# Optimization experiments

Hardware: AMD Instinct MI355X
Metric: run time of the kernel (lower is better)

## Reference

```python
import jax, jax.numpy as jnp
import numpy as np

N = 100000
E = 1600000
IN_DIM = 256
HID = 64


def setup_inputs() -> dict:
    key = jax.random.key(0)
    k1, k2, k3 = jax.random.split(key, 3)
    x = jax.random.normal(k1, (N, IN_DIM), dtype=jnp.float32)
    edge_index = jax.random.randint(k2, (2, E), 0, N, dtype=jnp.int64)
    # glorot-ish init for GCNConv weight, zero bias (PyG default)
    W = jax.random.normal(k3, (IN_DIM, HID), dtype=jnp.float32) * (1.0 / np.sqrt(IN_DIM))
    b = jnp.zeros((HID,), dtype=jnp.float32)
    return {"x": x, "edge_index": edge_index, "W": W, "b": b}


def reference(x, edge_index, W, b):
    # GCNConv: out = D^{-1/2} (A + I) D^{-1/2} (X W) + b
    n = x.shape[0]
    # add self-loops
    loop = jnp.arange(n, dtype=edge_index.dtype)
    src = jnp.concatenate([edge_index[0], loop])  # [E+N]
    dst = jnp.concatenate([edge_index[1], loop])  # [E+N]
    # degree of target nodes (incl. self-loops)
    deg = jax.ops.segment_sum(jnp.ones_like(dst, dtype=x.dtype), dst, num_segments=n)
    dinv = jnp.where(deg > 0, jax.lax.rsqrt(deg), 0.0)  # deg^{-1/2}, inf->0
    norm = dinv[src] * dinv[dst]  # [E+N]
    h = x @ W  # [N, HID] transform before aggregation
    msg = h[src] * norm[:, None]  # gather + scale, [E+N, HID]
    out = jax.ops.segment_sum(msg, dst, num_segments=n)  # scatter-add
    return out + b
```

## Files before the change

kernel.cpp:

```cpp
#include <hip/hip_runtime.h>

typedef float floatx4 __attribute__((ext_vector_type(4)));
typedef short s16x8 __attribute__((ext_vector_type(8)));

#define WG 256
#define NBUCK 512
#define BSH 8
#define EBLK 512
#define CAP 8192
#define MAXIT 16

__device__ inline unsigned pack_bf16_rne(float a, float b) {
    unsigned ua = __float_as_uint(a), ub = __float_as_uint(b);
    ua = (ua + 0x7FFFu + ((ua >> 16) & 1u)) >> 16;
    ub = (ub + 0x7FFFu + ((ub >> 16) & 1u)) >> 16;
    return ua | (ub << 16);
}

union FragU {
    unsigned u[4];
    uint4 q;
    s16x8 v;
};

__global__ __launch_bounds__(WG) void k_packw(const float* __restrict__ W,
                                              uint4* __restrict__ wpack,
                                              int* __restrict__ cursor) {
    const int q = blockIdx.x * WG + threadIdx.x;
    if (q < NBUCK) cursor[q] = 0;
    const int kb = q >> 8, nt = (q >> 6) & 3, ln = q & 63;
    const int quad = ln >> 4, l15 = ln & 15;
    const int col = nt * 16 + l15;
    const int krow = kb * 32 + quad * 8;
    unsigned up[4];
#pragma unroll
    for (int p = 0; p < 4; p++) {
        float a = W[(krow + 2 * p) * 64 + col];
        float b2 = W[(krow + 2 * p + 1) * 64 + col];
        up[p] = pack_bf16_rne(a, b2);
    }
    uint4 pk = {up[0], up[1], up[2], up[3]};
    wpack[q] = pk;
}

__global__ __launch_bounds__(WG, 4) void k_main(const void* __restrict__ ei, int* __restrict__ cursor,
                                                unsigned* __restrict__ ebuf, int E,
                                                const float* __restrict__ x, const uint4* __restrict__ wpack,
                                                unsigned short* __restrict__ g, int N) {
    __shared__ int hh[NBUCK];
    __shared__ int hbase[NBUCK];
    __shared__ int s32flag;
    const int t = threadIdx.x;

    if ((int)blockIdx.x < EBLK) {
        if (t == 0) s32flag = 0;
        for (int i = t; i < NBUCK; i += WG) hh[i] = 0;
        __syncthreads();
        {
            const int* w = (const int*)ei;
            int nz = 0;
            for (int j = t; j < 4096; j += WG) nz |= (w[2 * j + 1] != 0);
            if (nz) atomicOr(&s32flag, 1);
        }
        __syncthreads();
        const bool i32 = (s32flag != 0);
        const int chunk = (E + EBLK - 1) / EBLK;
        const int s = blockIdx.x * chunk;
        const int eend = min(E, s + chunk);

        if (chunk <= MAXIT * WG) {
            unsigned ew[MAXIT];
            unsigned short ebk[MAXIT];
#pragma unroll
            for (int i = 0; i < MAXIT; i++) {
                const int e = s + t + i * WG;
                ebk[i] = 0xFFFFu;
                if (e < eend) {
                    int sN, dN;
                    if (i32) {
                        const int* p = (const int*)ei;
                        sN = p[e];
                        dN = p[E + e];
                    } else {
                        const long long* p = (const long long*)ei;
                        sN = (int)p[e];
                        dN = (int)p[(long long)E + e];
                    }
                    ew[i] = (unsigned)sN | ((unsigned)(dN & 255) << 24);
                    ebk[i] = (unsigned short)(dN >> BSH);
                    atomicAdd(&hh[dN >> BSH], 1);
                }
            }
            __syncthreads();
            for (int i = t; i < NBUCK; i += WG) {
                int c = hh[i];
                hbase[i] = c ? atomicAdd(&cursor[i], c) : 0;
                hh[i] = 0;
            }
            __syncthreads();
#pragma unroll
            for (int i = 0; i < MAXIT; i++) {
                if (ebk[i] != 0xFFFFu) {
                    const int bkt = ebk[i];
                    const int pos = hbase[bkt] + atomicAdd(&hh[bkt], 1);
                    if (pos < CAP) ebuf[(size_t)bkt * CAP + pos] = ew[i];
                }
            }
        } else {
            if (i32) {
                const int* pd = (const int*)ei + E;
                for (int e = s + t; e < eend; e += WG) atomicAdd(&hh[pd[e] >> BSH], 1);
            } else {
                const long long* pd = (const long long*)ei + E;
                for (int e = s + t; e < eend; e += WG) atomicAdd(&hh[(int)pd[e] >> BSH], 1);
            }
            __syncthreads();
            for (int i = t; i < NBUCK; i += WG) {
                int c = hh[i];
                hbase[i] = c ? atomicAdd(&cursor[i], c) : 0;
                hh[i] = 0;
            }
            __syncthreads();
            for (int e = s + t; e < eend; e += WG) {
                int sN, dN;
                if (i32) {
                    const int* p = (const int*)ei;
                    sN = p[e];
                    dN = p[E + e];
                } else {
                    const long long* p = (const long long*)ei;
                    sN = (int)p[e];
                    dN = (int)p[(long long)E + e];
                }
                int bkt = dN >> BSH;
                int pos = hbase[bkt] + atomicAdd(&hh[bkt], 1);
                if (pos < CAP) ebuf[(size_t)bkt * CAP + pos] = (unsigned)sN | ((unsigned)(dN & 255) << 24);
            }
        }
    } else {
        const int bb = blockIdx.x - EBLK;
        const int wv = t >> 6;
        const int lane = t & 63;
        const int quad = lane >> 4, l15 = lane & 15;

        long long arow = (long long)bb * 64 + wv * 16 + l15;
        if (arow >= N) arow = N - 1;
        const float* xr = x + arow * 256 + quad * 8;
        const uint4* wp = wpack + lane;

        floatx4 xv[8][2];
#pragma unroll
        for (int kb = 0; kb < 8; kb++) {
            xv[kb][0] = *(const floatx4*)(xr + kb * 32);
            xv[kb][1] = *(const floatx4*)(xr + kb * 32 + 4);
        }
#pragma unroll
        for (int kb = 0; kb < 8; kb++) {
            asm volatile("" : "+v"(xv[kb][0]), "+v"(xv[kb][1]));
        }
        __builtin_amdgcn_sched_barrier(0);

        floatx4 acc[4];
#pragma unroll
        for (int nt = 0; nt < 4; nt++) acc[nt] = 0.f;

        FragU bc0, bc1, bc2, bc3;
        bc0.q = wp[0 * 64];
        bc1.q = wp[1 * 64];
        bc2.q = wp[2 * 64];
        bc3.q = wp[3 * 64];

#pragma unroll
        for (int kb = 0; kb < 8; kb++) {
            FragU bn0, bn1, bn2, bn3;
            if (kb < 7) {
                bn0.q = wp[((kb + 1) * 4 + 0) * 64];
                bn1.q = wp[((kb + 1) * 4 + 1) * 64];
                bn2.q = wp[((kb + 1) * 4 + 2) * 64];
                bn3.q = wp[((kb + 1) * 4 + 3) * 64];
            }
            FragU a;
            a.u[0] = pack_bf16_rne(xv[kb][0][0], xv[kb][0][1]);
            a.u[1] = pack_bf16_rne(xv[kb][0][2], xv[kb][0][3]);
            a.u[2] = pack_bf16_rne(xv[kb][1][0], xv[kb][1][1]);
            a.u[3] = pack_bf16_rne(xv[kb][1][2], xv[kb][1][3]);
            acc[0] = __builtin_amdgcn_mfma_f32_16x16x32_bf16(a.v, bc0.v, acc[0], 0, 0, 0);
            acc[1] = __builtin_amdgcn_mfma_f32_16x16x32_bf16(a.v, bc1.v, acc[1], 0, 0, 0);
            acc[2] = __builtin_amdgcn_mfma_f32_16x16x32_bf16(a.v, bc2.v, acc[2], 0, 0, 0);
            acc[3] = __builtin_amdgcn_mfma_f32_16x16x32_bf16(a.v, bc3.v, acc[3], 0, 0, 0);
            if (kb < 7) {
                bc0 = bn0;
                bc1 = bn1;
                bc2 = bn2;
                bc3 = bn3;
            }
        }

        const long long orow0 = (long long)bb * 64 + wv * 16 + quad * 4;
#pragma unroll
        for (int r = 0; r < 4; r++) {
            const long long orow = orow0 + r;
            if (orow < N) {
#pragma unroll
                for (int nt = 0; nt < 4; nt++) {
                    float v = acc[nt][r];
                    unsigned uv = __float_as_uint(v);
                    uv = (uv + 0x7FFFu + ((uv >> 16) & 1u)) >> 16;
                    g[orow * 64 + nt * 16 + l15] = (unsigned short)uv;
                }
            }
        }
    }
}

__global__ __launch_bounds__(WG) void k_csr(const unsigned* __restrict__ ebuf, const int* __restrict__ cursor,
                                            int* __restrict__ off, int* __restrict__ srcs,
                                            float* __restrict__ dinv, int N, int nbuse) {
    __shared__ int red[256];
    __shared__ int h[256];
    __shared__ int sc[256];
    __shared__ int cur[256];
    const int t = threadIdx.x;
    const int b = blockIdx.x;
    const int node0 = b << BSH;
    const int rows = min(256, N - node0);
    int part = 0;
    for (int i = t; i < b; i += WG) part += min(cursor[i], CAP);
    red[t] = part;
    h[t] = 0;
    __syncthreads();
    for (int d = WG / 2; d > 0; d >>= 1) {
        if (t < d) red[t] += red[t + d];
        __syncthreads();
    }
    const int ebase = red[0];
    const int cnt = min(cursor[b], CAP);
    const unsigned* eb = ebuf + (size_t)b * CAP;
    for (int j = t; j < cnt; j += WG) atomicAdd(&h[eb[j] >> 24], 1);
    __syncthreads();
    const int deg = (t < rows) ? h[t] + 1 : 0;
    sc[t] = deg;
    __syncthreads();
    for (int d = 1; d < 256; d <<= 1) {
        int a = (t >= d) ? sc[t - d] : 0;
        __syncthreads();
        sc[t] += a;
        __syncthreads();
    }
    const int basef = ebase + node0;
    const int local = sc[t] - deg;
    if (t < rows) {
        off[node0 + t] = basef + local;
        srcs[basef + local] = node0 + t;
        cur[t] = local + 1;
        dinv[node0 + t] = rsqrtf((float)deg);
    }
    if (b == nbuse - 1 && t == 0) off[N] = ebase + cnt + N;
    __syncthreads();
    for (int j = t; j < cnt; j += WG) {
        unsigned w = eb[j];
        int dl = (int)(w >> 24);
        int pos = basef + atomicAdd(&cur[dl], 1);
        srcs[pos] = (int)(w & 0xFFFFFFu);
    }
}

__global__ __launch_bounds__(WG) void k_gather(const unsigned short* __restrict__ g,
                                               const int* __restrict__ off, const int* __restrict__ srcs,
                                               const float* __restrict__ dinv, const float* __restrict__ bias,
                                               float* __restrict__ out, int N) {
    int wid = (blockIdx.x * WG + threadIdx.x) >> 6;
    int lane = threadIdx.x & 63;
    if (wid >= N) return;
    int grp = lane >> 3;
    int c8 = (lane & 7) * 8;
    int e0 = off[wid], e1 = off[wid + 1];
    float a0 = 0.f, a1 = 0.f, a2 = 0.f, a3 = 0.f, a4 = 0.f, a5 = 0.f, a6 = 0.f, a7 = 0.f;
    int e = e0 + grp;
    int s = (e < e1) ? srcs[e] : 0;
    while (e < e1) {
        int en = e + 8;
        int sn = (en < e1) ? srcs[en] : 0;
        float ds = dinv[s];
        uint4 v = *(const uint4*)(g + (long long)s * 64 + c8);
        a0 += ds * __uint_as_float(v.x << 16);
        a1 += ds * __uint_as_float(v.x & 0xFFFF0000u);
        a2 += ds * __uint_as_float(v.y << 16);
        a3 += ds * __uint_as_float(v.y & 0xFFFF0000u);
        a4 += ds * __uint_as_float(v.z << 16);
        a5 += ds * __uint_as_float(v.z & 0xFFFF0000u);
        a6 += ds * __uint_as_float(v.w << 16);
        a7 += ds * __uint_as_float(v.w & 0xFFFF0000u);
        s = sn;
        e = en;
    }
#pragma unroll
    for (int m = 8; m <= 32; m <<= 1) {
        a0 += __shfl_xor(a0, m, 64);
        a1 += __shfl_xor(a1, m, 64);
        a2 += __shfl_xor(a2, m, 64);
        a3 += __shfl_xor(a3, m, 64);
        a4 += __shfl_xor(a4, m, 64);
        a5 += __shfl_xor(a5, m, 64);
        a6 += __shfl_xor(a6, m, 64);
        a7 += __shfl_xor(a7, m, 64);
    }
    if (grp == 0) {
        float d = dinv[wid];
        const floatx4 b0 = *(const floatx4*)(bias + c8);
        const floatx4 b1 = *(const floatx4*)(bias + c8 + 4);
        floatx4 o0, o1;
        o0[0] = d * a0 + b0[0];
        o0[1] = d * a1 + b0[1];
        o0[2] = d * a2 + b0[2];
        o0[3] = d * a3 + b0[3];
        o1[0] = d * a4 + b1[0];
        o1[1] = d * a5 + b1[1];
        o1[2] = d * a6 + b1[2];
        o1[3] = d * a7 + b1[3];
        *(floatx4*)(out + (long long)wid * 64 + c8) = o0;
        *(floatx4*)(out + (long long)wid * 64 + c8 + 4) = o1;
    }
}

extern "C" void kernel_launch(void* const* d_in, const int* in_sizes, int n_in,
                              void* d_out, int out_size, void* d_ws, size_t ws_size,
                              hipStream_t stream) {
    const float* x = (const float*)d_in[0];
    const void* ei = d_in[1];
    const float* W = (const float*)d_in[2];
    const float* b = (const float*)d_in[3];
    float* out = (float*)d_out;

    const int N = in_sizes[0] / 256;
    const int E = in_sizes[1] / 2;
    const int NBUSE = (N + 255) >> BSH;
    const int GEMMB = (N + 63) / 64;

    char* ws = (char*)d_ws;
    size_t o = 0;
    auto alloc = [&](size_t bytes) -> void* {
        void* p = ws + o;
        o += (bytes + 255) & ~(size_t)255;
        return p;
    };
    float* dinv = (float*)alloc((size_t)N * 4);
    unsigned short* g = (unsigned short*)alloc((size_t)N * 64 * 2);
    unsigned* ebuf = (unsigned*)alloc((size_t)NBUSE * CAP * 4);
    int* cursor = (int*)alloc((size_t)NBUCK * 4);
    int* off = (int*)alloc((size_t)(N + 1) * 4);
    int* srcs = (int*)alloc((size_t)(E + N) * 4);
    uint4* wpack = (uint4*)alloc((size_t)2048 * 16);
    if (o > ws_size) return;

    k_packw<<<8, WG, 0, stream>>>(W, wpack, cursor);
    k_main<<<EBLK + GEMMB, WG, 0, stream>>>(ei, cursor, ebuf, E, x, wpack, g, N);
    k_csr<<<NBUSE, WG, 0, stream>>>(ebuf, cursor, off, srcs, dinv, N, NBUSE);
    k_gather<<<(N * 64 + WG - 1) / WG, WG, 0, stream>>>(g, off, srcs, dinv, b, out, N);
}
```

Baseline: 252.4 us.

## Split fused build/GEMM kernel, pad bucket cursors, remap gather to 8 lanes per node

The fused edge-bucketing plus GEMM kernel is split into two separate launches. The GEMM x loads become inline asm with a single waitcnt. Global bucket cursors are padded 16 ints apart so atomics on neighbouring buckets do not share cache lines. The gather kernel now assigns 8 lanes per node instead of a full wavefront, which removes the cross-lane shuffle reduction but walks each node's edges serially with less memory-level parallelism per node.

New measurement: 267.8 us. 1.06x slower.

```diff
diff --git a/kernel.cpp b/kernel.cpp
--- a/kernel.cpp
+++ b/kernel.cpp
@@ -9,6 +9,7 @@
 #define EBLK 512
 #define CAP 8192
 #define MAXIT 16
+#define CPAD 16
 
 __device__ inline unsigned pack_bf16_rne(float a, float b) {
     unsigned ua = __float_as_uint(a), ub = __float_as_uint(b);
@@ -27,7 +28,7 @@
                                               uint4* __restrict__ wpack,
                                               int* __restrict__ cursor) {
     const int q = blockIdx.x * WG + threadIdx.x;
-    if (q < NBUCK) cursor[q] = 0;
+    for (int z = q; z < NBUCK * CPAD; z += 2048) cursor[z] = 0;
     const int kb = q >> 8, nt = (q >> 6) & 3, ln = q & 63;
     const int quad = ln >> 4, l15 = ln & 15;
     const int col = nt * 16 + l15;
@@ -43,85 +44,35 @@
     wpack[q] = pk;
 }
 
-__global__ __launch_bounds__(WG, 4) void k_main(const void* __restrict__ ei, int* __restrict__ cursor,
-                                                unsigned* __restrict__ ebuf, int E,
-                                                const float* __restrict__ x, const uint4* __restrict__ wpack,
-                                                unsigned short* __restrict__ g, int N) {
+__global__ __launch_bounds__(WG) void k_build(const void* __restrict__ ei, int* __restrict__ cursor,
+                                              unsigned* __restrict__ ebuf, int E) {
     __shared__ int hh[NBUCK];
     __shared__ int hbase[NBUCK];
     __shared__ int s32flag;
     const int t = threadIdx.x;
-
-    if ((int)blockIdx.x < EBLK) {
-        if (t == 0) s32flag = 0;
-        for (int i = t; i < NBUCK; i += WG) hh[i] = 0;
-        __syncthreads();
-        {
-            const int* w = (const int*)ei;
-            int nz = 0;
-            for (int j = t; j < 4096; j += WG) nz |= (w[2 * j + 1] != 0);
-            if (nz) atomicOr(&s32flag, 1);
-        }
-        __syncthreads();
-        const bool i32 = (s32flag != 0);
-        const int chunk = (E + EBLK - 1) / EBLK;
-        const int s = blockIdx.x * chunk;
-        const int eend = min(E, s + chunk);
-
-        if (chunk <= MAXIT * WG) {
-            unsigned ew[MAXIT];
-            unsigned short ebk[MAXIT];
-#pragma unroll
-            for (int i = 0; i < MAXIT; i++) {
-                const int e = s + t + i * WG;
-                ebk[i] = 0xFFFFu;
-                if (e < eend) {
-                    int sN, dN;
-                    if (i32) {
-                        const int* p = (const int*)ei;
-                        sN = p[e];
-                        dN = p[E + e];
-                    } else {
-                        const long long* p = (const long long*)ei;
-                        sN = (int)p[e];
-                        dN = (int)p[(long long)E + e];
-                    }
-                    ew[i] = (unsigned)sN | ((unsigned)(dN & 255) << 24);
-                    ebk[i] = (unsigned short)(dN >> BSH);
-                    atomicAdd(&hh[dN >> BSH], 1);
-                }
-            }
-            __syncthreads();
-            for (int i = t; i < NBUCK; i += WG) {
-                int c = hh[i];
-                hbase[i] = c ? atomicAdd(&cursor[i], c) : 0;
-                hh[i] = 0;
-            }
-            __syncthreads();
-#pragma unroll
-            for (int i = 0; i < MAXIT; i++) {
-                if (ebk[i] != 0xFFFFu) {
-                    const int bkt = ebk[i];
-                    const int pos = hbase[bkt] + atomicAdd(&hh[bkt], 1);
-                    if (pos < CAP) ebuf[(size_t)bkt * CAP + pos] = ew[i];
-                }
-            }
-        } else {
-            if (i32) {
-                const int* pd = (const int*)ei + E;
-                for (int e = s + t; e < eend; e += WG) atomicAdd(&hh[pd[e] >> BSH], 1);
-            } else {
-                const long long* pd = (const long long*)ei + E;
-                for (int e = s + t; e < eend; e += WG) atomicAdd(&hh[(int)pd[e] >> BSH], 1);
-            }
-            __syncthreads();
-            for (int i = t; i < NBUCK; i += WG) {
-                int c = hh[i];
-                hbase[i] = c ? atomicAdd(&cursor[i], c) : 0;
-                hh[i] = 0;
-            }
-            __syncthreads();
-            for (int e = s + t; e < eend; e += WG) {
+    if (t == 0) s32flag = 0;
+    for (int i = t; i < NBUCK; i += WG) hh[i] = 0;
+    __syncthreads();
+    {
+        const int* w = (const int*)ei;
+        int nz = 0;
+        for (int j = t; j < 4096; j += WG) nz |= (w[2 * j + 1] != 0);
+        if (nz) atomicOr(&s32flag, 1);
+    }
+    __syncthreads();
+    const bool i32 = (s32flag != 0);
+    const int chunk = (E + EBLK - 1) / EBLK;
+    const int s = blockIdx.x * chunk;
+    const int eend = min(E, s + chunk);
+
+    if (chunk <= MAXIT * WG) {
+        unsigned ew[MAXIT];
+        unsigned short ebk[MAXIT];
+#pragma unroll
+        for (int i = 0; i < MAXIT; i++) {
+            const int e = s + t + i * WG;
+            ebk[i] = 0xFFFFu;
+            if (e < eend) {
                 int sN, dN;
                 if (i32) {
                     const int* p = (const int*)ei;
@@ -132,82 +83,135 @@
                     sN = (int)p[e];
                     dN = (int)p[(long long)E + e];
                 }
-                int bkt = dN >> BSH;
-                int pos = hbase[bkt] + atomicAdd(&hh[bkt], 1);
-                if (pos < CAP) ebuf[(size_t)bkt * CAP + pos] = (unsigned)sN | ((unsigned)(dN & 255) << 24);
+                ew[i] = (unsigned)sN | ((unsigned)(dN & 255) << 24);
+                ebk[i] = (unsigned short)(dN >> BSH);
+                atomicAdd(&hh[dN >> BSH], 1);
             }
         }
+        __syncthreads();
+        for (int i = t; i < NBUCK; i += WG) {
+            int c = hh[i];
+            hbase[i] = c ? atomicAdd(&cursor[i * CPAD], c) : 0;
+            hh[i] = 0;
+        }
+        __syncthreads();
+#pragma unroll
+        for (int i = 0; i < MAXIT; i++) {
+            if (ebk[i] != 0xFFFFu) {
+                const int bkt = ebk[i];
+                const int pos = hbase[bkt] + atomicAdd(&hh[bkt], 1);
+                if (pos < CAP) ebuf[(size_t)bkt * CAP + pos] = ew[i];
+            }
+        }
     } else {
-        const int bb = blockIdx.x - EBLK;
-        const int wv = t >> 6;
-        const int lane = t & 63;
-        const int quad = lane >> 4, l15 = lane & 15;
-
-        long long arow = (long long)bb * 64 + wv * 16 + l15;
-        if (arow >= N) arow = N - 1;
-        const float* xr = x + arow * 256 + quad * 8;
-        const uint4* wp = wpack + lane;
-
-        floatx4 xv[8][2];
-#pragma unroll
-        for (int kb = 0; kb < 8; kb++) {
-            xv[kb][0] = *(const floatx4*)(xr + kb * 32);
-            xv[kb][1] = *(const floatx4*)(xr + kb * 32 + 4);
-        }
-#pragma unroll
-        for (int kb = 0; kb < 8; kb++) {
-            asm volatile("" : "+v"(xv[kb][0]), "+v"(xv[kb][1]));
-        }
-        __builtin_amdgcn_sched_barrier(0);
-
-        floatx4 acc[4];
-#pragma unroll
-        for (int nt = 0; nt < 4; nt++) acc[nt] = 0.f;
-
-        FragU bc0, bc1, bc2, bc3;
-        bc0.q = wp[0 * 64];
-        bc1.q = wp[1 * 64];
-        bc2.q = wp[2 * 64];
-        bc3.q = wp[3 * 64];
-
-#pragma unroll
-        for (int kb = 0; kb < 8; kb++) {
-            FragU bn0, bn1, bn2, bn3;
-            if (kb < 7) {
-                bn0.q = wp[((kb + 1) * 4 + 0) * 64];
-                bn1.q = wp[((kb + 1) * 4 + 1) * 64];
-                bn2.q = wp[((kb + 1) * 4 + 2) * 64];
-                bn3.q = wp[((kb + 1) * 4 + 3) * 64];
+        if (i32) {
+            const int* pd = (const int*)ei + E;
+            for (int e = s + t; e < eend; e += WG) atomicAdd(&hh[pd[e] >> BSH], 1);
+        } else {
+            const long long* pd = (const long long*)ei + E;
+            for (int e = s + t; e < eend; e += WG) atomicAdd(&hh[(int)pd[e] >> BSH], 1);
+        }
+        __syncthreads();
+        for (int i = t; i < NBUCK; i += WG) {
+            int c = hh[i];
+            hbase[i] = c ? atomicAdd(&cursor[i * CPAD], c) : 0;
+            hh[i] = 0;
+        }
+        __syncthreads();
+        for (int e = s + t; e < eend; e += WG) {
+            int sN, dN;
+            if (i32) {
+                const int* p = (const int*)ei;
+                sN = p[e];
+                dN = p[E + e];
+            } else {
+                const long long* p = (const long long*)ei;
+                sN = (int)p[e];
+                dN = (int)p[(long long)E + e];
             }
-            FragU a;
-            a.u[0] = pack_bf16_rne(xv[kb][0][0], xv[kb][0][1]);
-            a.u[1] = pack_bf16_rne(xv[kb][0][2], xv[kb][0][3]);
-            a.u[2] = pack_bf16_rne(xv[kb][1][0], xv[kb][1][1]);
-            a.u[3] = pack_bf16_rne(xv[kb][1][2], xv[kb][1][3]);
-            acc[0] = __builtin_amdgcn_mfma_f32_16x16x32_bf16(a.v, bc0.v, acc[0], 0, 0, 0);
-            acc[1] = __builtin_amdgcn_mfma_f32_16x16x32_bf16(a.v, bc1.v, acc[1], 0, 0, 0);
-            acc[2] = __builtin_amdgcn_mfma_f32_16x16x32_bf16(a.v, bc2.v, acc[2], 0, 0, 0);
-            acc[3] = __builtin_amdgcn_mfma_f32_16x16x32_bf16(a.v, bc3.v, acc[3], 0, 0, 0);
-            if (kb < 7) {
-                bc0 = bn0;
-                bc1 = bn1;
-                bc2 = bn2;
-                bc3 = bn3;
-            }
-        }
-
-        const long long orow0 = (long long)bb * 64 + wv * 16 + quad * 4;
-#pragma unroll
-        for (int r = 0; r < 4; r++) {
-            const long long orow = orow0 + r;
-            if (orow < N) {
-#pragma unroll
-                for (int nt = 0; nt < 4; nt++) {
-                    float v = acc[nt][r];
-                    unsigned uv = __float_as_uint(v);
-                    uv = (uv + 0x7FFFu + ((uv >> 16) & 1u)) >> 16;
-                    g[orow * 64 + nt * 16 + l15] = (unsigned short)uv;
-                }
+            int bkt = dN >> BSH;
+            int pos = hbase[bkt] + atomicAdd(&hh[bkt], 1);
+            if (pos < CAP) ebuf[(size_t)bkt * CAP + pos] = (unsigned)sN | ((unsigned)(dN & 255) << 24);
+        }
+    }
+}
+
+__global__ __launch_bounds__(WG, 4) void k_gemm(const float* __restrict__ x, const uint4* __restrict__ wpack,
+                                                unsigned short* __restrict__ g, int N) {
+    const int t = threadIdx.x;
+    const int bb = blockIdx.x;
+    const int wv = t >> 6;
+    const int lane = t & 63;
+    const int quad = lane >> 4, l15 = lane & 15;
+
+    long long arow = (long long)bb * 64 + wv * 16 + l15;
+    if (arow >= N) arow = N - 1;
+    const float* xr = x + arow * 256 + quad * 8;
+    const uint4* wp = wpack + lane;
+
+    floatx4 xv[8][2];
+#pragma unroll
+    for (int kb = 0; kb < 8; kb++) {
+        const float* p = xr + kb * 32;
+        asm volatile("global_load_dwordx4 %0, %2, off\n\t"
+                     "global_load_dwordx4 %1, %2, off offset:16"
+                     : "=&v"(xv[kb][0]), "=&v"(xv[kb][1])
+                     : "v"(p));
+    }
+    asm volatile("s_waitcnt vmcnt(0)"
+                 : "+v"(xv[0][0]), "+v"(xv[0][1]), "+v"(xv[1][0]), "+v"(xv[1][1]),
+                   "+v"(xv[2][0]), "+v"(xv[2][1]), "+v"(xv[3][0]), "+v"(xv[3][1]),
+                   "+v"(xv[4][0]), "+v"(xv[4][1]), "+v"(xv[5][0]), "+v"(xv[5][1]),
+                   "+v"(xv[6][0]), "+v"(xv[6][1]), "+v"(xv[7][0]), "+v"(xv[7][1]));
+    __builtin_amdgcn_sched_barrier(0);
+
+    floatx4 acc[4];
+#pragma unroll
+    for (int nt = 0; nt < 4; nt++) acc[nt] = 0.f;
+
+    FragU bc0, bc1, bc2, bc3;
+    bc0.q = wp[0 * 64];
+    bc1.q = wp[1 * 64];
+    bc2.q = wp[2 * 64];
+    bc3.q = wp[3 * 64];
+
+#pragma unroll
+    for (int kb = 0; kb < 8; kb++) {
+        FragU bn0, bn1, bn2, bn3;
+        if (kb < 7) {
+            bn0.q = wp[((kb + 1) * 4 + 0) * 64];
+            bn1.q = wp[((kb + 1) * 4 + 1) * 64];
+            bn2.q = wp[((kb + 1) * 4 + 2) * 64];
+            bn3.q = wp[((kb + 1) * 4 + 3) * 64];
+        }
+        FragU a;
+        a.u[0] = pack_bf16_rne(xv[kb][0][0], xv[kb][0][1]);
+        a.u[1] = pack_bf16_rne(xv[kb][0][2], xv[kb][0][3]);
+        a.u[2] = pack_bf16_rne(xv[kb][1][0], xv[kb][1][1]);
+        a.u[3] = pack_bf16_rne(xv[kb][1][2], xv[kb][1][3]);
+        acc[0] = __builtin_amdgcn_mfma_f32_16x16x32_bf16(a.v, bc0.v, acc[0], 0, 0, 0);
+        acc[1] = __builtin_amdgcn_mfma_f32_16x16x32_bf16(a.v, bc1.v, acc[1], 0, 0, 0);
+        acc[2] = __builtin_amdgcn_mfma_f32_16x16x32_bf16(a.v, bc2.v, acc[2], 0, 0, 0);
+        acc[3] = __builtin_amdgcn_mfma_f32_16x16x32_bf16(a.v, bc3.v, acc[3], 0, 0, 0);
+        if (kb < 7) {
+            bc0 = bn0;
+            bc1 = bn1;
+            bc2 = bn2;
+            bc3 = bn3;
+        }
+    }
+
+    const long long orow0 = (long long)bb * 64 + wv * 16 + quad * 4;
+#pragma unroll
+    for (int r = 0; r < 4; r++) {
+        const long long orow = orow0 + r;
+        if (orow < N) {
+#pragma unroll
+            for (int nt = 0; nt < 4; nt++) {
+                float v = acc[nt][r];
+                unsigned uv = __float_as_uint(v);
+                uv = (uv + 0x7FFFu + ((uv >> 16) & 1u)) >> 16;
+                g[orow * 64 + nt * 16 + l15] = (unsigned short)uv;
             }
         }
     }
@@ -225,7 +229,7 @@
     const int node0 = b << BSH;
     const int rows = min(256, N - node0);
     int part = 0;
-    for (int i = t; i < b; i += WG) part += min(cursor[i], CAP);
+    for (int i = t; i < b; i += WG) part += min(cursor[i * CPAD], CAP);
     red[t] = part;
     h[t] = 0;
     __syncthreads();
@@ -234,7 +238,7 @@
         __syncthreads();
     }
     const int ebase = red[0];
-    const int cnt = min(cursor[b], CAP);
+    const int cnt = min(cursor[b * CPAD], CAP);
     const unsigned* eb = ebuf + (size_t)b * CAP;
     for (int j = t; j < cnt; j += WG) atomicAdd(&h[eb[j] >> 24], 1);
     __syncthreads();
@@ -269,20 +273,19 @@
                                                const int* __restrict__ off, const int* __restrict__ srcs,
                                                const float* __restrict__ dinv, const float* __restrict__ bias,
                                                float* __restrict__ out, int N) {
-    int wid = (blockIdx.x * WG + threadIdx.x) >> 6;
-    int lane = threadIdx.x & 63;
-    if (wid >= N) return;
-    int grp = lane >> 3;
-    int c8 = (lane & 7) * 8;
-    int e0 = off[wid], e1 = off[wid + 1];
+    const int t = threadIdx.x;
+    const int node = blockIdx.x * 32 + (t >> 3);
+    if (node >= N) return;
+    const int c8 = (t & 7) * 8;
+    const int e1 = off[node + 1];
+    int e = off[node];
     float a0 = 0.f, a1 = 0.f, a2 = 0.f, a3 = 0.f, a4 = 0.f, a5 = 0.f, a6 = 0.f, a7 = 0.f;
-    int e = e0 + grp;
-    int s = (e < e1) ? srcs[e] : 0;
+    int s = srcs[e];
     while (e < e1) {
-        int en = e + 8;
-        int sn = (en < e1) ? srcs[en] : 0;
-        float ds = dinv[s];
-        uint4 v = *(const uint4*)(g + (long long)s * 64 + c8);
+        const int en = e + 1;
+        const int sn = (en < e1) ? srcs[en] : 0;
+        const float ds = dinv[s];
+        const uint4 v = *(const uint4*)(g + (long long)s * 64 + c8);
         a0 += ds * __uint_as_float(v.x << 16);
         a1 += ds * __uint_as_float(v.x & 0xFFFF0000u);
         a2 += ds * __uint_as_float(v.y << 16);
@@ -294,33 +297,20 @@
         s = sn;
         e = en;
     }
-#pragma unroll
-    for (int m = 8; m <= 32; m <<= 1) {
-        a0 += __shfl_xor(a0, m, 64);
-        a1 += __shfl_xor(a1, m, 64);
-        a2 += __shfl_xor(a2, m, 64);
-        a3 += __shfl_xor(a3, m, 64);
-        a4 += __shfl_xor(a4, m, 64);
-        a5 += __shfl_xor(a5, m, 64);
-        a6 += __shfl_xor(a6, m, 64);
-        a7 += __shfl_xor(a7, m, 64);
-    }
-    if (grp == 0) {
-        float d = dinv[wid];
-        const floatx4 b0 = *(const floatx4*)(bias + c8);
-        const floatx4 b1 = *(const floatx4*)(bias + c8 + 4);
-        floatx4 o0, o1;
-        o0[0] = d * a0 + b0[0];
-        o0[1] = d * a1 + b0[1];
-        o0[2] = d * a2 + b0[2];
-        o0[3] = d * a3 + b0[3];
-        o1[0] = d * a4 + b1[0];
-        o1[1] = d * a5 + b1[1];
-        o1[2] = d * a6 + b1[2];
-        o1[3] = d * a7 + b1[3];
-        *(floatx4*)(out + (long long)wid * 64 + c8) = o0;
-        *(floatx4*)(out + (long long)wid * 64 + c8 + 4) = o1;
-    }
+    const float d = dinv[node];
+    const floatx4 b0 = *(const floatx4*)(bias + c8);
+    const floatx4 b1 = *(const floatx4*)(bias + c8 + 4);
+    floatx4 o0, o1;
+    o0[0] = d * a0 + b0[0];
+    o0[1] = d * a1 + b0[1];
+    o0[2] = d * a2 + b0[2];
+    o0[3] = d * a3 + b0[3];
+    o1[0] = d * a4 + b1[0];
+    o1[1] = d * a5 + b1[1];
+    o1[2] = d * a6 + b1[2];
+    o1[3] = d * a7 + b1[3];
+    *(floatx4*)(out + (long long)node * 64 + c8) = o0;
+    *(floatx4*)(out + (long long)node * 64 + c8 + 4) = o1;
 }
 
 extern "C" void kernel_launch(void* const* d_in, const int* in_sizes, int n_in,
@@ -347,14 +337,15 @@
     float* dinv = (float*)alloc((size_t)N * 4);
     unsigned short* g = (unsigned short*)alloc((size_t)N * 64 * 2);
     unsigned* ebuf = (unsigned*)alloc((size_t)NBUSE * CAP * 4);
-    int* cursor = (int*)alloc((size_t)NBUCK * 4);
+    int* cursor = (int*)alloc((size_t)NBUCK * CPAD * 4);
     int* off = (int*)alloc((size_t)(N + 1) * 4);
     int* srcs = (int*)alloc((size_t)(E + N) * 4);
     uint4* wpack = (uint4*)alloc((size_t)2048 * 16);
     if (o > ws_size) return;
 
     k_packw<<<8, WG, 0, stream>>>(W, wpack, cursor);
-    k_main<<<EBLK + GEMMB, WG, 0, stream>>>(ei, cursor, ebuf, E, x, wpack, g, N);
+    k_build<<<EBLK, WG, 0, stream>>>(ei, cursor, ebuf, E);
+    k_gemm<<<GEMMB, WG, 0, stream>>>(x, wpack, g, N);
     k_csr<<<NBUSE, WG, 0, stream>>>(ebuf, cursor, off, srcs, dinv, N, NBUSE);
-    k_gather<<<(N * 64 + WG - 1) / WG, WG, 0, stream>>>(g, off, srcs, dinv, b, out, N);
-}
+    k_gather<<<(N + 31) / 32, WG, 0, stream>>>(g, off, srcs, dinv, b, out, N);
+}
```
